# Performance work log

Measured on AMD Instinct MI355X. Metric: run time of the kernel, lower is better.

## Reference

```python
import jax, jax.numpy as jnp
import numpy as np

D_MODEL = 1024
NHEAD = 16
D_K = D_MODEL // NHEAD


def setup_inputs() -> dict:
    key = jax.random.key(0)
    ks = jax.random.split(key, 9)
    s = 1.0 / np.sqrt(D_MODEL)
    return {
        "x": jax.random.normal(ks[0], (4, 2048, D_MODEL), dtype=jnp.float32),
        "Wq": jax.random.uniform(ks[1], (D_MODEL, D_MODEL), jnp.float32, -s, s),
        "bq": jax.random.uniform(ks[2], (D_MODEL,), jnp.float32, -s, s),
        "Wk": jax.random.uniform(ks[3], (D_MODEL, D_MODEL), jnp.float32, -s, s),
        "bk": jax.random.uniform(ks[4], (D_MODEL,), jnp.float32, -s, s),
        "Wv": jax.random.uniform(ks[5], (D_MODEL, D_MODEL), jnp.float32, -s, s),
        "bv": jax.random.uniform(ks[6], (D_MODEL,), jnp.float32, -s, s),
        "Wo": jax.random.uniform(ks[7], (D_MODEL, D_MODEL), jnp.float32, -s, s),
        "bo": jax.random.uniform(ks[8], (D_MODEL,), jnp.float32, -s, s),
    }


def reference(x, Wq, bq, Wk, bk, Wv, bv, Wo, bo):
    B, S, D = x.shape
    H, dk = NHEAD, D_K

    def split_heads(t):  # [B,S,D] -> [B,H,S,dk]
        return t.reshape(B, S, H, dk).transpose(0, 2, 1, 3)

    q = split_heads(x @ Wq + bq)
    k = split_heads(x @ Wk + bk)
    v = split_heads(x @ Wv + bv)

    scores = jnp.einsum('bhqd,bhkd->bhqk', q, k) / jnp.sqrt(jnp.float32(dk))
    attn = jax.nn.softmax(scores, axis=-1)
    out = jnp.einsum('bhqk,bhkd->bhqd', attn, v)  # [B,H,S,dk]
    out = out.transpose(0, 2, 1, 3).reshape(B, S, D)
    return out @ Wo + bo
```

## Files before the change

### kernel.cpp

```cpp
#include <hip/hip_runtime.h>


typedef short short8 __attribute__((ext_vector_type(8)));
typedef float f32x4 __attribute__((ext_vector_type(4)));
typedef float f32x16 __attribute__((ext_vector_type(16)));

#define DMODEL 1024
#define NH 16
#define DK 64
#define SEQ 2048
#define NB 4
#define MTOT (NB*SEQ)
#define KSCALE 0.18033688f

__device__ __forceinline__ unsigned short f2bf(float f) {
    union { float f; unsigned u; } v; v.f = f;
    unsigned r = (v.u + 0x7FFFu + ((v.u >> 16) & 1u)) >> 16;
    return (unsigned short)r;
}

__device__ __forceinline__ unsigned pk2(float a, float b) {
    unsigned r;
    asm("v_cvt_pk_bf16_f32 %0, %1, %2" : "=v"(r) : "v"(a), "v"(b));
    return r;
}

__device__ __forceinline__ float exp2a(float x) {
    float r; asm("v_exp_f32 %0, %1" : "=v"(r) : "v"(x)); return r;
}

__device__ __forceinline__ float max3a(float a, float b, float c) {
    float r; asm("v_max3_f32 %0, %1, %2, %3" : "=v"(r) : "v"(a), "v"(b), "v"(c)); return r;
}

__device__ __forceinline__ void plswap(unsigned &a, unsigned &b) {
    asm volatile("v_permlane32_swap_b32 %0, %1" : "+v"(a), "+v"(b));
}

__device__ __forceinline__ void gload16(const short* g, short* l) {
    __builtin_amdgcn_global_load_lds(
        (const __attribute__((address_space(1))) unsigned*)(const void*)g,
        (__attribute__((address_space(3))) unsigned*)(void*)l,
        16, 0, 0);
}

__device__ __forceinline__ void vm4()   { asm volatile("s_waitcnt vmcnt(4)"   ::: "memory"); }
__device__ __forceinline__ void vm0()   { asm volatile("s_waitcnt vmcnt(0)"   ::: "memory"); }
__device__ __forceinline__ void lgkm0() { asm volatile("s_waitcnt lgkmcnt(0)" ::: "memory"); }

union Frag { short8 s8; unsigned u[4]; };

#define NCVT (MTOT * DMODEL / 4 / 256)
__global__ __launch_bounds__(256) void prep_kernel(
    const float* __restrict__ x, short* __restrict__ xb,
    const float* __restrict__ Wq, const float* __restrict__ Wk,
    const float* __restrict__ Wv, const float* __restrict__ Wo,
    short* __restrict__ Wqkvt, short* __restrict__ Wot)
{
    __shared__ float t[32][33];
    int bid = blockIdx.x;
    if (bid < NCVT) {
        int i = bid * 256 + threadIdx.x;
        float4 v = ((const float4*)x)[i];
        short4 o;
        o.x = (short)f2bf(v.x); o.y = (short)f2bf(v.y);
        o.z = (short)f2bf(v.z); o.w = (short)f2bf(v.w);
        ((short4*)xb)[i] = o;
        return;
    }
    int wb = bid - NCVT;
    int widx = wb >> 10, tile = wb & 1023;
    const float* W = (widx == 0) ? Wq : (widx == 1) ? Wk : (widx == 2) ? Wv : Wo;
    short* dst = (widx < 3) ? (Wqkvt + (size_t)widx * DMODEL * DMODEL) : Wot;
    int r0 = (tile >> 5) * 32, c0 = (tile & 31) * 32;
    int tr = threadIdx.x >> 3;
    int tc = (threadIdx.x & 7) * 4;
    float4 v = *(const float4*)&W[(r0 + tr) * DMODEL + c0 + tc];
    t[tr][tc + 0] = v.x; t[tr][tc + 1] = v.y; t[tr][tc + 2] = v.z; t[tr][tc + 3] = v.w;
    __syncthreads();
    short4 o;
    o.x = (short)f2bf(t[tc + 0][tr]);
    o.y = (short)f2bf(t[tc + 1][tr]);
    o.z = (short)f2bf(t[tc + 2][tr]);
    o.w = (short)f2bf(t[tc + 3][tr]);
    *(short4*)&dst[(c0 + tr) * DMODEL + r0 + tc] = o;
}

template<int MODE>
__global__ __launch_bounds__(256) void gemm_kernel(
    const short* __restrict__ A, const short* __restrict__ Bt,
    const float* __restrict__ b0, const float* __restrict__ b1, const float* __restrict__ b2,
    short* __restrict__ Qb, short* __restrict__ Kb, short* __restrict__ Vtb,
    float* __restrict__ Cout)
{
    __shared__ __align__(16) short L[3][2][128 * 32];
    const int K = DMODEL;
    const int NHP = 2 * (K / 64);
    int m0 = blockIdx.y * 128, n0 = blockIdx.x * 128;
    int tid = threadIdx.x, lane = tid & 63, wid = tid >> 6;
    int wm = (wid >> 1) * 64, wn = (wid & 1) * 64;

    int srowl = (lane >> 2);
    int scoll = ((lane & 3) ^ ((lane >> 3) & 3)) * 8;
    const short* aSrc = A + (size_t)(m0 + wid * 32 + srowl) * K + scoll;
    const short* bSrc = Bt + (size_t)(n0 + wid * 32 + srowl) * K + scoll;

    f32x4 acc[4][4];
    #pragma unroll
    for (int i = 0; i < 4; i++)
        #pragma unroll
        for (int j = 0; j < 4; j++) acc[i][j] = (f32x4){0.f, 0.f, 0.f, 0.f};

    auto STAGE = [&](int H) {
        int sl = H % 3;
        const short* as = aSrc + H * 32;
        const short* bs = bSrc + H * 32;
        #pragma unroll
        for (int i = 0; i < 2; ++i) {
            gload16(as + (size_t)i * 16 * K, &L[sl][0][(wid * 32 + i * 16) * 32]);
            gload16(bs + (size_t)i * 16 * K, &L[sl][1][(wid * 32 + i * 16) * 32]);
        }
    };
    auto LDA = [&](int sl, short8* f) {
        #pragma unroll
        for (int m = 0; m < 4; m++) {
            int r = wm + m * 16 + (lane & 15);
            f[m] = *(const short8*)&L[sl][0][r * 32 + (((lane >> 4) ^ ((r >> 1) & 3)) * 8)];
        }
    };
    auto LDB = [&](int sl, short8* f) {
        #pragma unroll
        for (int n = 0; n < 4; n++) {
            int r = wn + n * 16 + (lane & 15);
            f[n] = *(const short8*)&L[sl][1][r * 32 + (((lane >> 4) ^ ((r >> 1) & 3)) * 8)];
        }
    };

    STAGE(0);
    STAGE(1);
    vm4();
    __builtin_amdgcn_s_barrier();

    for (int H = 0; H < NHP; ++H) {
        int sl = H % 3;
        short8 af[4], bfv[4];
        LDA(sl, af); LDB(sl, bfv);
        if (H + 2 < NHP) STAGE(H + 2);
        lgkm0();
        __builtin_amdgcn_s_barrier();
        __builtin_amdgcn_s_setprio(1);
        #pragma unroll
        for (int i = 0; i < 4; i++)
            #pragma unroll
            for (int j = 0; j < 4; j++)
                acc[i][j] = __builtin_amdgcn_mfma_f32_16x16x32_bf16(af[i], bfv[j], acc[i][j], 0, 0, 0);
        __builtin_amdgcn_s_setprio(0);
        if (H + 2 < NHP)       { vm4(); __builtin_amdgcn_s_barrier(); }
        else if (H + 2 == NHP) { vm0(); __builtin_amdgcn_s_barrier(); }
    }

    #pragma unroll
    for (int i = 0; i < 4; i++) {
        #pragma unroll
        for (int j = 0; j < 4; j++) {
            int col = n0 + wn + j * 16 + (lane & 15);
            #pragma unroll
            for (int r = 0; r < 4; r++) {
                int row = m0 + wm + i * 16 + (lane >> 4) * 4 + r;
                float v = acc[i][j][r];
                if (MODE == 0) {
                    int seg = col >> 10, c = col & 1023;
                    const float* bp = (seg == 0) ? b0 : (seg == 1 ? b1 : b2);
                    v += bp[c];
                    if (seg == 1) v *= KSCALE;
                    unsigned short bv = f2bf(v);
                    int hh = c >> 6, d = c & 63, bb = row >> 11, s = row & 2047;
                    if (seg == 0)      Qb [(((bb * NH + hh) * SEQ) + s) * DK + d] = (short)bv;
                    else if (seg == 1) Kb [(((bb * NH + hh) * SEQ) + s) * DK + d] = (short)bv;
                    else               Vtb[(((bb * NH + hh) * DK) + d) * SEQ + s] = (short)bv;
                } else {
                    Cout[row * DMODEL + col] = v + b0[col];
                }
            }
        }
    }
}

__global__ __launch_bounds__(256) void attn_kernel(
    const short* __restrict__ Qb, const short* __restrict__ Kb,
    const short* __restrict__ Vtb, short* __restrict__ AOb)
{
    __shared__ __align__(16) short Ks[64 * 64];
    __shared__ __align__(16) short Vs[64 * 64];
    char* ksb = (char*)Ks;
    char* vsb = (char*)Vs;

    int bid = blockIdx.x;
    int wk = (bid & 7) * 128 + (bid >> 3);
    int qi = wk & 15, bh = wk >> 4;
    int h = bh & (NH - 1), b = bh >> 4;
    int q0 = qi * 128;

    int tid = threadIdx.x, lane = tid & 63, wid = tid >> 6;
    int hi = lane >> 5, l31 = lane & 31, l7 = lane & 7;
    const short* Qp = Qb + (size_t)bh * SEQ * DK;
    const short* Kp = Kb + (size_t)bh * SEQ * DK;
    const short* Vp = Vtb + (size_t)bh * DK * SEQ;

    short8 qf[4];
    #pragma unroll
    for (int ks = 0; ks < 4; ks++)
        qf[ks] = *(const short8*)&Qp[(q0 + wid * 32 + l31) * DK + ks * 16 + hi * 8];

    f32x16 ot0, ot1;
    #pragma unroll
    for (int r = 0; r < 16; r++) { ot0[r] = 0.f; ot1[r] = 0.f; }
    float mrun = -1e30f, lrun = 0.f;

    int srow = tid >> 3, ssl = tid & 7;
    #pragma unroll
    for (int i = 0; i < 2; i++) {
        int row = srow + 32 * i;
        *(short8*)(ksb + ((row * 128 + ssl * 16) ^ ((row & 7) << 4))) =
            *(const short8*)&Kp[row * DK + ssl * 8];
        *(short8*)(vsb + ((row * 128 + ssl * 16) ^ ((row & 7) << 4))) =
            *(const short8*)&Vp[row * SEQ + ssl * 8];
    }
    __syncthreads();

    const int NT = SEQ / 64;
    for (int t = 0; t < NT; ++t) {
        short8 nk[2], nv[2];
        if (t + 1 < NT) {
            int kv0n = (t + 1) * 64;
            #pragma unroll
            for (int i = 0; i < 2; i++) {
                int row = srow + 32 * i;
                nk[i] = *(const short8*)&Kp[(kv0n + row) * DK + ssl * 8];
                nv[i] = *(const short8*)&Vp[row * SEQ + kv0n + ssl * 8];
            }
        }

        f32x16 st0, st1;
        #pragma unroll
        for (int r = 0; r < 16; r++) { st0[r] = 0.f; st1[r] = 0.f; }
        __builtin_amdgcn_s_setprio(1);
        #pragma unroll
        for (int ks = 0; ks < 4; ks++) {
            short8 kf0 = *(const short8*)(ksb + ((l31 * 128 + ks * 32 + hi * 16) ^ (l7 << 4)));
            short8 kf1 = *(const short8*)(ksb + (((32 + l31) * 128 + ks * 32 + hi * 16) ^ (l7 << 4)));
            st0 = __builtin_amdgcn_mfma_f32_32x32x16_bf16(kf0, qf[ks], st0, 0, 0, 0);
            st1 = __builtin_amdgcn_mfma_f32_32x32x16_bf16(kf1, qf[ks], st1, 0, 0, 0);
        }
        __builtin_amdgcn_s_setprio(0);

        float m8[8];
        #pragma unroll
        for (int i = 0; i < 8; i++) m8[i] = max3a(st0[i], st0[i + 8], st1[i]);
        float m4[4];
        #pragma unroll
        for (int i = 0; i < 4; i++) m4[i] = max3a(m8[i], m8[i + 4], st1[i + 8]);
        float m2a = max3a(m4[0], m4[2], st1[12]);
        float m2b = max3a(m4[1], m4[3], st1[13]);
        float mxv = max3a(m2a, m2b, st1[14]);
        mxv = fmaxf(mxv, st1[15]);
        float mt = fmaxf(mxv, __shfl_xor(mxv, 32, 64));

        if (!__all(mt - mrun <= 11.0f)) {
            float mn = fmaxf(mrun, mt);
            float al = exp2a(mrun - mn);
            lrun *= al;
            #pragma unroll
            for (int r = 0; r < 16; r++) { ot0[r] *= al; ot1[r] *= al; }
            mrun = mn;
        }
        #pragma unroll
        for (int r = 0; r < 16; r++) {
            st0[r] = exp2a(st0[r] - mrun);
            st1[r] = exp2a(st1[r] - mrun);
        }
        float s16[16];
        #pragma unroll
        for (int r = 0; r < 16; r++) s16[r] = st0[r] + st1[r];
        #pragma unroll
        for (int s = 8; s > 0; s >>= 1)
            #pragma unroll
            for (int r = 0; r < 8; r++) if (r < s) s16[r] += s16[r + s];
        lrun += s16[0] + __shfl_xor(s16[0], 32, 64);

        unsigned w0[8], w1[8];
        #pragma unroll
        for (int m = 0; m < 4; m++) {
            w0[m * 2]     = pk2(st0[4 * m], st0[4 * m + 1]);
            w0[m * 2 + 1] = pk2(st0[4 * m + 2], st0[4 * m + 3]);
            w1[m * 2]     = pk2(st1[4 * m], st1[4 * m + 1]);
            w1[m * 2 + 1] = pk2(st1[4 * m + 2], st1[4 * m + 3]);
        }
        short8 pf[4];
        #pragma unroll
        for (int ks = 0; ks < 4; ks++) {
            unsigned a0 = (ks < 2) ? w0[4 * (ks & 1) + 0] : w1[4 * (ks & 1) + 0];
            unsigned b0_ = (ks < 2) ? w0[4 * (ks & 1) + 2] : w1[4 * (ks & 1) + 2];
            unsigned a1 = (ks < 2) ? w0[4 * (ks & 1) + 1] : w1[4 * (ks & 1) + 1];
            unsigned b1_ = (ks < 2) ? w0[4 * (ks & 1) + 3] : w1[4 * (ks & 1) + 3];
            plswap(a0, b0_);
            plswap(a1, b1_);
            Frag f;
            f.u[0] = a0; f.u[1] = a1; f.u[2] = b0_; f.u[3] = b1_;
            pf[ks] = f.s8;
        }

        __builtin_amdgcn_s_setprio(1);
        #pragma unroll
        for (int ks = 0; ks < 4; ks++) {
            short8 vf0 = *(const short8*)(vsb + ((l31 * 128 + ks * 32 + hi * 16) ^ (l7 << 4)));
            short8 vf1 = *(const short8*)(vsb + (((32 + l31) * 128 + ks * 32 + hi * 16) ^ (l7 << 4)));
            ot0 = __builtin_amdgcn_mfma_f32_32x32x16_bf16(vf0, pf[ks], ot0, 0, 0, 0);
            ot1 = __builtin_amdgcn_mfma_f32_32x32x16_bf16(vf1, pf[ks], ot1, 0, 0, 0);
        }
        __builtin_amdgcn_s_setprio(0);

        __syncthreads();
        if (t + 1 < NT) {
            #pragma unroll
            for (int i = 0; i < 2; i++) {
                int row = srow + 32 * i;
                *(short8*)(ksb + ((row * 128 + ssl * 16) ^ ((row & 7) << 4))) = nk[i];
                *(short8*)(vsb + ((row * 128 + ssl * 16) ^ ((row & 7) << 4))) = nv[i];
            }
        }
        __syncthreads();
    }

    float inv = 1.f / lrun;
    int srow_q = b * SEQ + q0 + wid * 32 + l31;
    short* outp = AOb + (size_t)srow_q * DMODEL + h * DK;
    #pragma unroll
    for (int g = 0; g < 4; g++) {
        int d0 = 8 * g + 4 * hi;
        uint2 u;
        u.x = pk2(ot0[4 * g] * inv, ot0[4 * g + 1] * inv);
        u.y = pk2(ot0[4 * g + 2] * inv, ot0[4 * g + 3] * inv);
        *(uint2*)&outp[d0] = u;
        uint2 v2;
        v2.x = pk2(ot1[4 * g] * inv, ot1[4 * g + 1] * inv);
        v2.y = pk2(ot1[4 * g + 2] * inv, ot1[4 * g + 3] * inv);
        *(uint2*)&outp[32 + d0] = v2;
    }
}

extern "C" void kernel_launch(void* const* d_in, const int* in_sizes, int n_in,
                              void* d_out, int out_size, void* d_ws, size_t ws_size,
                              hipStream_t stream)
{
    const float* x  = (const float*)d_in[0];
    const float* Wq = (const float*)d_in[1];
    const float* bq = (const float*)d_in[2];
    const float* Wk = (const float*)d_in[3];
    const float* bk = (const float*)d_in[4];
    const float* Wv = (const float*)d_in[5];
    const float* bv = (const float*)d_in[6];
    const float* Wo = (const float*)d_in[7];
    const float* bo = (const float*)d_in[8];
    float* out = (float*)d_out;

    char* w = (char*)d_ws;
    short* xb    = (short*)w; w += (size_t)MTOT * DMODEL * 2;
    short* Wqkvt = (short*)w; w += (size_t)3 * DMODEL * DMODEL * 2;
    short* Wot   = (short*)w; w += (size_t)DMODEL * DMODEL * 2;
    short* Qb    = (short*)w; w += (size_t)MTOT * DMODEL * 2;
    short* Kb    = (short*)w; w += (size_t)MTOT * DMODEL * 2;
    short* Vtb   = (short*)w; w += (size_t)MTOT * DMODEL * 2;
    short* AOb   = (short*)w; w += (size_t)MTOT * DMODEL * 2;

    prep_kernel<<<NCVT + 4096, 256, 0, stream>>>(x, xb, Wq, Wk, Wv, Wo, Wqkvt, Wot);

    gemm_kernel<0><<<dim3(3 * DMODEL / 128, MTOT / 128), 256, 0, stream>>>(
        xb, Wqkvt, bq, bk, bv, Qb, Kb, Vtb, nullptr);

    attn_kernel<<<dim3(SEQ / 128 * NH * NB), 256, 0, stream>>>(Qb, Kb, Vtb, AOb);

    gemm_kernel<1><<<dim3(DMODEL / 128, MTOT / 128), 256, 0, stream>>>(
        AOb, Wot, bo, nullptr, nullptr, nullptr, nullptr, nullptr, out);
}
```

Before: 219.9 us.

## Double-buffer GEMM fragments and fold softmax max/sum into MFMA

The GEMM main loop now double-buffers the A/B register fragments. It prefetches the next stage's LDS reads before the current MFMAs and uses partial lgkmcnt waits plus a reordered barrier scheme. In attention, the running-max subtraction is folded into the QK accumulator initialisation, and the row sum is computed by an extra MFMA against a ones vector instead of a VALU reduction and shuffle. This moves work from VALU to the matrix unit. The cost is one extra MFMA per k-step, and the row-sum denominator is now accumulated from bf16-rounded probabilities.

After: 238.5 us. 8.4% more time.

```diff
diff --git a/kernel.cpp b/kernel.cpp
--- a/kernel.cpp
+++ b/kernel.cpp
@@ -44,9 +44,10 @@
         16, 0, 0);
 }
 
-__device__ __forceinline__ void vm4()   { asm volatile("s_waitcnt vmcnt(4)"   ::: "memory"); }
-__device__ __forceinline__ void vm0()   { asm volatile("s_waitcnt vmcnt(0)"   ::: "memory"); }
-__device__ __forceinline__ void lgkm0() { asm volatile("s_waitcnt lgkmcnt(0)" ::: "memory"); }
+__device__ __forceinline__ void vm4()    { asm volatile("s_waitcnt vmcnt(4)"    ::: "memory"); }
+__device__ __forceinline__ void vm0()    { asm volatile("s_waitcnt vmcnt(0)"    ::: "memory"); }
+__device__ __forceinline__ void lgkm8()  { asm volatile("s_waitcnt lgkmcnt(8)"  ::: "memory"); }
+__device__ __forceinline__ void lgkm0()  { asm volatile("s_waitcnt lgkmcnt(0)"  ::: "memory"); }
 
 union Frag { short8 s8; unsigned u[4]; };
 
@@ -136,27 +137,37 @@
         }
     };
 
+    short8 fa0[4], fb0[4], fa1[4], fb1[4];
+
     STAGE(0);
     STAGE(1);
     vm4();
     __builtin_amdgcn_s_barrier();
-
+    LDA(0, fa0); LDB(0, fb0);
+
+    #pragma unroll
     for (int H = 0; H < NHP; ++H) {
-        int sl = H % 3;
-        short8 af[4], bfv[4];
-        LDA(sl, af); LDB(sl, bfv);
-        if (H + 2 < NHP) STAGE(H + 2);
-        lgkm0();
+        short8* curA = (H & 1) ? fa1 : fa0;
+        short8* curB = (H & 1) ? fb1 : fb0;
+        short8* nxtA = (H & 1) ? fa0 : fa1;
+        short8* nxtB = (H & 1) ? fb0 : fb1;
+
+        if (H + 2 < NHP) { STAGE(H + 2); vm4(); }
+        else             { vm0(); }
         __builtin_amdgcn_s_barrier();
+
+        if (H + 1 < NHP) { LDA((H + 1) % 3, nxtA); LDB((H + 1) % 3, nxtB); lgkm8(); }
+        else             { lgkm0(); }
+        __builtin_amdgcn_s_barrier();
+        __builtin_amdgcn_sched_barrier(0);
+
         __builtin_amdgcn_s_setprio(1);
         #pragma unroll
         for (int i = 0; i < 4; i++)
             #pragma unroll
             for (int j = 0; j < 4; j++)
-                acc[i][j] = __builtin_amdgcn_mfma_f32_16x16x32_bf16(af[i], bfv[j], acc[i][j], 0, 0, 0);
+                acc[i][j] = __builtin_amdgcn_mfma_f32_16x16x32_bf16(curA[i], curB[j], acc[i][j], 0, 0, 0);
         __builtin_amdgcn_s_setprio(0);
-        if (H + 2 < NHP)       { vm4(); __builtin_amdgcn_s_barrier(); }
-        else if (H + 2 == NHP) { vm0(); __builtin_amdgcn_s_barrier(); }
     }
 
     #pragma unroll
@@ -212,10 +223,15 @@
     for (int ks = 0; ks < 4; ks++)
         qf[ks] = *(const short8*)&Qp[(q0 + wid * 32 + l31) * DK + ks * 16 + hi * 8];
 
-    f32x16 ot0, ot1;
-    #pragma unroll
-    for (int r = 0; r < 16; r++) { ot0[r] = 0.f; ot1[r] = 0.f; }
-    float mrun = -1e30f, lrun = 0.f;
+    Frag onef;
+    onef.u[0] = 0x3F803F80u; onef.u[1] = 0x3F803F80u;
+    onef.u[2] = 0x3F803F80u; onef.u[3] = 0x3F803F80u;
+    short8 onesv = onef.s8;
+
+    f32x16 ot0, ot1, ot2;
+    #pragma unroll
+    for (int r = 0; r < 16; r++) { ot0[r] = 0.f; ot1[r] = 0.f; ot2[r] = 0.f; }
+    float mrun = 0.f;
 
     int srow = tid >> 3, ssl = tid & 7;
     #pragma unroll
@@ -241,9 +257,10 @@
             }
         }
 
+        float negm = -mrun;
         f32x16 st0, st1;
         #pragma unroll
-        for (int r = 0; r < 16; r++) { st0[r] = 0.f; st1[r] = 0.f; }
+        for (int r = 0; r < 16; r++) { st0[r] = negm; st1[r] = negm; }
         __builtin_amdgcn_s_setprio(1);
         #pragma unroll
         for (int ks = 0; ks < 4; ks++) {
@@ -266,27 +283,22 @@
         mxv = fmaxf(mxv, st1[15]);
         float mt = fmaxf(mxv, __shfl_xor(mxv, 32, 64));
 
-        if (!__all(mt - mrun <= 11.0f)) {
-            float mn = fmaxf(mrun, mt);
-            float al = exp2a(mrun - mn);
-            lrun *= al;
-            #pragma unroll
-            for (int r = 0; r < 16; r++) { ot0[r] *= al; ot1[r] *= al; }
-            mrun = mn;
+        if (!__all(mt <= 11.0f)) {
+            float d = fmaxf(mt, 0.f);
+            float al = exp2a(-d);
+            ot2[0] *= al;
+            #pragma unroll
+            for (int r = 0; r < 16; r++) {
+                ot0[r] *= al; ot1[r] *= al;
+                st0[r] -= d; st1[r] -= d;
+            }
+            mrun += d;
         }
         #pragma unroll
         for (int r = 0; r < 16; r++) {
-            st0[r] = exp2a(st0[r] - mrun);
-            st1[r] = exp2a(st1[r] - mrun);
-        }
-        float s16[16];
-        #pragma unroll
-        for (int r = 0; r < 16; r++) s16[r] = st0[r] + st1[r];
-        #pragma unroll
-        for (int s = 8; s > 0; s >>= 1)
-            #pragma unroll
-            for (int r = 0; r < 8; r++) if (r < s) s16[r] += s16[r + s];
-        lrun += s16[0] + __shfl_xor(s16[0], 32, 64);
+            st0[r] = exp2a(st0[r]);
+            st1[r] = exp2a(st1[r]);
+        }
 
         unsigned w0[8], w1[8];
         #pragma unroll
@@ -317,6 +329,7 @@
             short8 vf1 = *(const short8*)(vsb + (((32 + l31) * 128 + ks * 32 + hi * 16) ^ (l7 << 4)));
             ot0 = __builtin_amdgcn_mfma_f32_32x32x16_bf16(vf0, pf[ks], ot0, 0, 0, 0);
             ot1 = __builtin_amdgcn_mfma_f32_32x32x16_bf16(vf1, pf[ks], ot1, 0, 0, 0);
+            ot2 = __builtin_amdgcn_mfma_f32_32x32x16_bf16(onesv, pf[ks], ot2, 0, 0, 0);
         }
         __builtin_amdgcn_s_setprio(0);
 
@@ -332,7 +345,7 @@
         __syncthreads();
     }
 
-    float inv = 1.f / lrun;
+    float inv = 1.f / ot2[0];
     int srow_q = b * SEQ + q0 + wid * 32 + l31;
     short* outp = AOb + (size_t)srow_q * DMODEL + h * DK;
     #pragma unroll
```

## Double-buffer LDS fragments in GEMM and use async direct-to-LDS K/V loads in attention

Applied to the files above, without the earlier changes.

In the GEMM kernel, the fragments for the next K-step are loaded from LDS into a second register set while the current step's MFMAs run, with finer-grained lgkmcnt waits. In the attention kernel, the K/V staging is double-buffered in LDS and uses global_load_lds, replacing the register round-trip and the extra barrier. The swizzle is now applied on the global-address side. Both changes aim to hide LDS and global latency behind MFMA work, at the cost of more registers and more LDS, and the attention path no longer waits on vmcnt explicitly before reading the next buffer.

After: 227.3 us. +3.4%, slower.

```diff
diff --git a/kernel.cpp b/kernel.cpp
--- a/kernel.cpp
+++ b/kernel.cpp
@@ -44,9 +44,10 @@
         16, 0, 0);
 }
 
-__device__ __forceinline__ void vm4()   { asm volatile("s_waitcnt vmcnt(4)"   ::: "memory"); }
-__device__ __forceinline__ void vm0()   { asm volatile("s_waitcnt vmcnt(0)"   ::: "memory"); }
-__device__ __forceinline__ void lgkm0() { asm volatile("s_waitcnt lgkmcnt(0)" ::: "memory"); }
+__device__ __forceinline__ void vm4()    { asm volatile("s_waitcnt vmcnt(4)"    ::: "memory"); }
+__device__ __forceinline__ void vm0()    { asm volatile("s_waitcnt vmcnt(0)"    ::: "memory"); }
+__device__ __forceinline__ void lgkm8()  { asm volatile("s_waitcnt lgkmcnt(8)"  ::: "memory"); }
+__device__ __forceinline__ void lgkm0()  { asm volatile("s_waitcnt lgkmcnt(0)"  ::: "memory"); }
 
 union Frag { short8 s8; unsigned u[4]; };
 
@@ -136,27 +137,37 @@
         }
     };
 
+    short8 fa0[4], fb0[4], fa1[4], fb1[4];
+
     STAGE(0);
     STAGE(1);
     vm4();
     __builtin_amdgcn_s_barrier();
-
+    LDA(0, fa0); LDB(0, fb0);
+
+    #pragma unroll
     for (int H = 0; H < NHP; ++H) {
-        int sl = H % 3;
-        short8 af[4], bfv[4];
-        LDA(sl, af); LDB(sl, bfv);
-        if (H + 2 < NHP) STAGE(H + 2);
-        lgkm0();
+        short8* curA = (H & 1) ? fa1 : fa0;
+        short8* curB = (H & 1) ? fb1 : fb0;
+        short8* nxtA = (H & 1) ? fa0 : fa1;
+        short8* nxtB = (H & 1) ? fb0 : fb1;
+
+        if (H + 2 < NHP) { STAGE(H + 2); vm4(); }
+        else             { vm0(); }
         __builtin_amdgcn_s_barrier();
+
+        if (H + 1 < NHP) { LDA((H + 1) % 3, nxtA); LDB((H + 1) % 3, nxtB); lgkm8(); }
+        else             { lgkm0(); }
+        __builtin_amdgcn_s_barrier();
+        __builtin_amdgcn_sched_barrier(0);
+
         __builtin_amdgcn_s_setprio(1);
         #pragma unroll
         for (int i = 0; i < 4; i++)
             #pragma unroll
             for (int j = 0; j < 4; j++)
-                acc[i][j] = __builtin_amdgcn_mfma_f32_16x16x32_bf16(af[i], bfv[j], acc[i][j], 0, 0, 0);
+                acc[i][j] = __builtin_amdgcn_mfma_f32_16x16x32_bf16(curA[i], curB[j], acc[i][j], 0, 0, 0);
         __builtin_amdgcn_s_setprio(0);
-        if (H + 2 < NHP)       { vm4(); __builtin_amdgcn_s_barrier(); }
-        else if (H + 2 == NHP) { vm0(); __builtin_amdgcn_s_barrier(); }
     }
 
     #pragma unroll
@@ -190,10 +201,8 @@
     const short* __restrict__ Qb, const short* __restrict__ Kb,
     const short* __restrict__ Vtb, short* __restrict__ AOb)
 {
-    __shared__ __align__(16) short Ks[64 * 64];
-    __shared__ __align__(16) short Vs[64 * 64];
-    char* ksb = (char*)Ks;
-    char* vsb = (char*)Vs;
+    __shared__ __align__(16) short Ks[2][64 * 64];
+    __shared__ __align__(16) short Vs[2][64 * 64];
 
     int bid = blockIdx.x;
     int wk = (bid & 7) * 128 + (bid >> 3);
@@ -207,6 +216,11 @@
     const short* Kp = Kb + (size_t)bh * SEQ * DK;
     const short* Vp = Vtb + (size_t)bh * DK * SEQ;
 
+    int srow = 8 * wid + (lane >> 3);
+    int scol = ((lane & 7) ^ (lane >> 3)) * 8;
+    const short* kS = Kp + (size_t)srow * DK + scol;
+    const short* vS = Vp + (size_t)srow * SEQ + scol;
+
     short8 qf[4];
     #pragma unroll
     for (int ks = 0; ks < 4; ks++)
@@ -217,27 +231,26 @@
     for (int r = 0; r < 16; r++) { ot0[r] = 0.f; ot1[r] = 0.f; }
     float mrun = -1e30f, lrun = 0.f;
 
-    int srow = tid >> 3, ssl = tid & 7;
     #pragma unroll
     for (int i = 0; i < 2; i++) {
-        int row = srow + 32 * i;
-        *(short8*)(ksb + ((row * 128 + ssl * 16) ^ ((row & 7) << 4))) =
-            *(const short8*)&Kp[row * DK + ssl * 8];
-        *(short8*)(vsb + ((row * 128 + ssl * 16) ^ ((row & 7) << 4))) =
-            *(const short8*)&Vp[row * SEQ + ssl * 8];
+        gload16(kS + (size_t)(32 * i) * DK, &Ks[0][(8 * wid + 32 * i) * 64]);
+        gload16(vS + (size_t)(32 * i) * SEQ, &Vs[0][(8 * wid + 32 * i) * 64]);
     }
     __syncthreads();
 
     const int NT = SEQ / 64;
     for (int t = 0; t < NT; ++t) {
-        short8 nk[2], nv[2];
+        int cur = t & 1, nb = cur ^ 1;
+        const char* ksb = (const char*)Ks[cur];
+        const char* vsb = (const char*)Vs[cur];
+
         if (t + 1 < NT) {
-            int kv0n = (t + 1) * 64;
             #pragma unroll
             for (int i = 0; i < 2; i++) {
-                int row = srow + 32 * i;
-                nk[i] = *(const short8*)&Kp[(kv0n + row) * DK + ssl * 8];
-                nv[i] = *(const short8*)&Vp[row * SEQ + kv0n + ssl * 8];
+                gload16(kS + (size_t)((t + 1) * 64 + 32 * i) * DK,
+                        &Ks[nb][(8 * wid + 32 * i) * 64]);
+                gload16(vS + (size_t)(32 * i) * SEQ + (t + 1) * 64,
+                        &Vs[nb][(8 * wid + 32 * i) * 64]);
             }
         }
 
@@ -320,15 +333,6 @@
         }
         __builtin_amdgcn_s_setprio(0);
 
-        __syncthreads();
-        if (t + 1 < NT) {
-            #pragma unroll
-            for (int i = 0; i < 2; i++) {
-                int row = srow + 32 * i;
-                *(short8*)(ksb + ((row * 128 + ssl * 16) ^ ((row & 7) << 4))) = nk[i];
-                *(short8*)(vsb + ((row * 128 + ssl * 16) ^ ((row & 7) << 4))) = nv[i];
-            }
-        }
         __syncthreads();
     }
 
```
